# Optimization experiments

Hardware: AMD Instinct MI355X
Metric: run time of the kernel (lower is better)

The kernel has to match this reference:

```python
import jax, jax.numpy as jnp
import numpy as np

AZ = -999999.0  # ALMOST_ZERO_LOG_SCALE
N = 100000      # nodes
E = N - 1       # tree edges
D = 768         # input_dim
H = 256         # hidden_dim
C = 16          # num_classes


def setup_inputs() -> dict:
    key = jax.random.key(0)
    ks = jax.random.split(key, 14)
    scale = 0.02
    features = jax.random.normal(ks[0], (N, D), dtype=jnp.float32)
    # tree edges: child i (1..N-1) has parent sampled from [0, N)
    parent_idx = jax.random.randint(ks[1], (E,), 0, N, dtype=jnp.int32)
    child_idx = jnp.arange(1, N, dtype=jnp.int32)
    label_observed = jax.random.randint(ks[2], (N,), 0, 2, dtype=jnp.int32)
    true_labels = jax.random.randint(ks[3], (N,), 0, C, dtype=jnp.int32)
    # MLP feature extractor (num_layers=2, Linear+ReLU each, feature_extractor=True)
    W1 = jax.random.normal(ks[4], (D, H), dtype=jnp.float32) * scale
    b1 = jnp.zeros((H,), dtype=jnp.float32)
    W2 = jax.random.normal(ks[5], (H, H), dtype=jnp.float32) * scale
    b2 = jnp.zeros((H,), dtype=jnp.float32)
    # build_unary_potentials: Linear(H, C)
    Wu = jax.random.normal(ks[6], (H, C), dtype=jnp.float32) * scale
    bu = jnp.zeros((C,), dtype=jnp.float32)
    # build_edge_potentials: Linear(2H, C*C)
    We = jax.random.normal(ks[7], (2 * H, C * C), dtype=jnp.float32) * scale
    be = jnp.zeros((C * C,), dtype=jnp.float32)
    return {
        "features": features, "parent_idx": parent_idx, "child_idx": child_idx,
        "label_observed": label_observed, "true_labels": true_labels,
        "W1": W1, "b1": b1, "W2": W2, "b2": b2,
        "Wu": Wu, "bu": bu, "We": We, "be": be,
    }


def reference(features, parent_idx, child_idx, label_observed, true_labels,
              W1, b1, W2, b2, Wu, bu, We, be):
    obs = label_observed.astype(bool)
    # MLP feature extractor over all nodes at once (original loops per-node)
    h = jax.nn.relu(features @ W1 + b1)
    h = jax.nn.relu(h @ W2 + b2)                      # [N, H]
    # unary potentials; observed nodes get 0 at true label, AZ elsewhere
    unary_pred = h @ Wu + bu                          # [N, C]
    lbl = jnp.arange(C, dtype=true_labels.dtype)
    obs_unary = jnp.where(true_labels[:, None] == lbl[None, :], 0.0, AZ)
    unary = jnp.where(obs[:, None], obs_unary, unary_pred)  # [N, C]
    # edge potentials: Linear on concat(parent_hidden, child_hidden)
    hp = h[parent_idx]                                # [E, H]
    hc = h[child_idx]                                 # [E, H]
    ep = (jnp.concatenate([hp, hc], axis=1) @ We + be).reshape(E, C, C)
    pl = true_labels[parent_idx]                      # [E]
    cl = true_labels[child_idx]                       # [E]
    op = obs[parent_idx]                              # [E]
    oc = obs[child_idx]                               # [E]
    row = lbl[None, :, None]                          # broadcast over rows
    col = lbl[None, None, :]                          # broadcast over cols
    # both observed: 0 at [parent_label, child_label], AZ elsewhere
    allow_both = (row == pl[:, None, None]) & (col == cl[:, None, None])
    both = (op & oc)[:, None, None]
    # child-only observed: keep row at child label; parent-only: keep col at parent label
    keep = (((oc & ~op)[:, None, None] & (row == cl[:, None, None]))
            | ((op & ~oc)[:, None, None] & (col == pl[:, None, None]))
            | (~op & ~oc)[:, None, None])
    ep_masked = jnp.where(both,
                          jnp.where(allow_both, 0.0, AZ),
                          jnp.where(keep, ep, ep + AZ))
    return unary, ep_masked
```

## Files before the change

kernel.cpp:

```cpp
#include <hip/hip_runtime.h>
#include <cstddef>

#define AZ -999999.0f

typedef float  f32x4  __attribute__((ext_vector_type(4)));
typedef short  s16x8  __attribute__((ext_vector_type(8)));
typedef __bf16 bf16x8 __attribute__((ext_vector_type(8)));
typedef unsigned short ushort_t;

__device__ __forceinline__ ushort_t f2bf(float f) {
    return __builtin_bit_cast(ushort_t, (__bf16)f);
}

__device__ __forceinline__ f32x4 mfma16(s16x8 a, s16x8 b, f32x4 c) {
    return __builtin_amdgcn_mfma_f32_16x16x32_bf16(
        __builtin_bit_cast(bf16x8, a), __builtin_bit_cast(bf16x8, b), c, 0, 0, 0);
}

__device__ __forceinline__ void gl2lds16(const void* g, void* l) {
    __builtin_amdgcn_global_load_lds(
        (const __attribute__((address_space(1))) unsigned int*)g,
        (__attribute__((address_space(3))) unsigned int*)l, 16, 0, 0);
}

__global__ void setup_kernel(
    const float* __restrict__ W1, const float* __restrict__ W2,
    const float* __restrict__ We, const float* __restrict__ Wu,
    ushort_t* __restrict__ W1T, ushort_t* __restrict__ W2T,
    ushort_t* __restrict__ WeT, ushort_t* __restrict__ WuTs,
    const int* __restrict__ pidx, const int* __restrict__ cidx,
    const int* __restrict__ tl, const int* __restrict__ obs,
    int* __restrict__ meta, int E)
{
    int b = blockIdx.x, t = threadIdx.x;
    if (b < 768) {
        int idx = b * 256 + t; int k = idx >> 8, n = idx & 255;
        W1T[(size_t)n * 768 + k] = f2bf(W1[idx]);
    } else if (b < 1024) {
        int idx = (b - 768) * 256 + t; int k = idx >> 8, n = idx & 255;
        W2T[n * 256 + k] = f2bf(W2[idx]);
    } else if (b < 1536) {
        int idx = (b - 1024) * 256 + t; int k = idx >> 8, n = idx & 255;
        WeT[(size_t)n * 512 + k] = f2bf(We[idx]);
    } else if (b < 1552) {
        int idx = (b - 1536) * 256 + t; int k = idx >> 4, c = idx & 15;
        WuTs[c * 256 + (((k >> 3) ^ (c & 7)) << 3) + (k & 7)] = f2bf(Wu[idx]);
    } else {
        int e = (b - 1552) * 256 + t;
        if (e < E) {
            int p = pidx[e], c = cidx[e];
            meta[e] = (tl[p] & 15) | ((tl[c] & 15) << 4)
                    | ((obs[p] & 1) << 8) | ((obs[c] & 1) << 9);
        }
    }
}

template<int AMODE, int EPI>
__global__ __launch_bounds__(256) void gemm_kernel(
    const void* __restrict__ Aptr, const ushort_t* __restrict__ BT,
    const float* __restrict__ bias, void* __restrict__ outp,
    int M, int K,
    const int* __restrict__ parent_idx, const int* __restrict__ child_idx,
    const int* __restrict__ meta)
{
    constexpr int ABYTES = (AMODE == 0) ? 8192 : 4096;
    __shared__ __align__(16) char smem[ABYTES + 16384];
    float*    Asf = (float*)smem;
    ushort_t* Ash = (ushort_t*)smem;
    ushort_t* Bsh = (ushort_t*)(smem + ABYTES);

    const int tid  = threadIdx.x;
    const int lane = tid & 63, wave = tid >> 6;
    const int row0 = blockIdx.y * 64;
    const int wc   = wave * 64;
    const int quad = lane >> 4, l16 = lane & 15;
    const int c4   = lane & 3;

    const int rB  = tid >> 2;
    const int gcB = c4 ^ ((rB >> 1) & 3);
    size_t   b_off[4]; unsigned lds_b[4];
#pragma unroll
    for (int j = 0; j < 4; ++j) {
        b_off[j] = (size_t)(j * 64 + rB) * K + gcB * 8;
        lds_b[j] = (unsigned)(j * 64 + wave * 16) * 64;
    }

    size_t a_off[2]; unsigned lds_a[2];
    int pn = 0, cn = 0; unsigned lds_a0 = 0, a_col = 0;
    if constexpr (AMODE == 0) {
        const int c8 = tid & 7, r8 = tid >> 3;
        const int gcA = c8 ^ (r8 & 7);
#pragma unroll
        for (int j = 0; j < 2; ++j) {
            int gr = row0 + j * 32 + r8; if (gr > M - 1) gr = M - 1;
            a_off[j] = (size_t)gr * K + gcA * 4;
            lds_a[j] = (unsigned)(j * 32 + wave * 8) * 128;
        }
    } else {
        const int rA = tid >> 2;
        const int gcA2 = c4 ^ ((rA >> 1) & 3);
        int gr = row0 + rA; if (gr > M - 1) gr = M - 1;
        pn = parent_idx[gr]; cn = child_idx[gr];
        a_col  = gcA2 * 8;
        lds_a0 = (unsigned)(wave * 16) * 64;
    }

    const f32x4 fz = {0.f, 0.f, 0.f, 0.f};
    f32x4 acc[4][4];
#pragma unroll
    for (int i = 0; i < 4; ++i)
#pragma unroll
        for (int j = 0; j < 4; ++j) acc[i][j] = fz;

    const ushort_t* Abh = (const ushort_t*)Aptr;
    const float*    Af  = (const float*)Aptr;

    const int nkt = K >> 5;
    for (int kt = 0; kt < nkt; ++kt) {
        const int kbase = kt << 5;
        if constexpr (AMODE == 0) {
#pragma unroll
            for (int j = 0; j < 2; ++j)
                gl2lds16(Af + a_off[j] + kbase, smem + lds_a[j]);
        } else {
            int node = (kbase < 256) ? pn : cn;
            gl2lds16(Abh + (size_t)node * 256 + (kbase & 255) + a_col,
                     smem + lds_a0);
        }
#pragma unroll
        for (int j = 0; j < 4; ++j)
            gl2lds16(BT + b_off[j] + kbase, (char*)Bsh + lds_b[j]);

        __syncthreads();

        s16x8 af[4], bf[4];
        if constexpr (AMODE == 0) {
            const int s = l16 & 7;
            const int c0 = (2 * quad) ^ s, c1 = c0 ^ 1;
#pragma unroll
            for (int f = 0; f < 4; ++f) {
                int row = f * 16 + l16;
                f32x4 v0 = *(const f32x4*)&Asf[row * 32 + c0 * 4];
                f32x4 v1 = *(const f32x4*)&Asf[row * 32 + c1 * 4];
                s16x8 a;
                a[0] = (short)f2bf(v0[0]); a[1] = (short)f2bf(v0[1]);
                a[2] = (short)f2bf(v0[2]); a[3] = (short)f2bf(v0[3]);
                a[4] = (short)f2bf(v1[0]); a[5] = (short)f2bf(v1[1]);
                a[6] = (short)f2bf(v1[2]); a[7] = (short)f2bf(v1[3]);
                af[f] = a;
            }
        } else {
            const int ca = quad ^ ((l16 >> 1) & 3);
#pragma unroll
            for (int f = 0; f < 4; ++f)
                af[f] = *(const s16x8*)&Ash[(f * 16 + l16) * 32 + ca * 8];
        }
        {
            const int cb = quad ^ ((l16 >> 1) & 3);
#pragma unroll
            for (int f = 0; f < 4; ++f)
                bf[f] = *(const s16x8*)&Bsh[(wc + f * 16 + l16) * 32 + cb * 8];
        }
#pragma unroll
        for (int fr = 0; fr < 4; ++fr)
#pragma unroll
            for (int fc = 0; fc < 4; ++fc)
                acc[fr][fc] = mfma16(af[fr], bf[fc], acc[fr][fc]);
        __syncthreads();
    }

    float bv[4];
#pragma unroll
    for (int fc = 0; fc < 4; ++fc) bv[fc] = bias[wc + fc * 16 + l16];

    if constexpr (EPI == 0) {
        ushort_t* out = (ushort_t*)outp;
#pragma unroll
        for (int fr = 0; fr < 4; ++fr) {
#pragma unroll
            for (int r = 0; r < 4; ++r) {
                int gr = row0 + fr * 16 + quad * 4 + r;
                if (gr < M) {
#pragma unroll
                    for (int fc = 0; fc < 4; ++fc) {
                        float v = acc[fr][fc][r] + bv[fc];
                        v = v > 0.f ? v : 0.f;
                        out[(size_t)gr * 256 + wc + fc * 16 + l16] = f2bf(v);
                    }
                }
            }
        }
    } else {
        float* out = (float*)outp;
#pragma unroll
        for (int fr = 0; fr < 4; ++fr) {
#pragma unroll
            for (int r = 0; r < 4; ++r) {
                int e = row0 + fr * 16 + quad * 4 + r;
                if (e < M) {
                    int m  = meta[e];
                    int pl = m & 15, cl = (m >> 4) & 15;
                    int op = (m >> 8) & 1, oc = (m >> 9) & 1;
#pragma unroll
                    for (int fc = 0; fc < 4; ++fc) {
                        int n = wc + fc * 16 + l16;
                        float v = acc[fr][fc][r] + bv[fc];
                        int rr = n >> 4, cc = n & 15;
                        if (op & oc)  v = (rr == pl && cc == cl) ? 0.0f : AZ;
                        else if (oc)  { if (rr != cl) v += AZ; }
                        else if (op)  { if (cc != pl) v += AZ; }
                        out[(size_t)e * 256 + n] = v;
                    }
                }
            }
        }
    }
}

__global__ __launch_bounds__(256) void gemm2_unary_kernel(
    const ushort_t* __restrict__ h1, const ushort_t* __restrict__ W2T,
    const float* __restrict__ b2, const ushort_t* __restrict__ WuTs,
    const float* __restrict__ bu, const int* __restrict__ tl,
    const int* __restrict__ obs, ushort_t* __restrict__ h2,
    float* __restrict__ out_unary, int N)
{
    __shared__ __align__(16) char smem[4096 + 16384 + 32768 + 8192];
    ushort_t* Ash = (ushort_t*)smem;
    ushort_t* Bsh = (ushort_t*)(smem + 4096);
    ushort_t* Hsh = (ushort_t*)(smem + 20480);
    ushort_t* Wsh = (ushort_t*)(smem + 53248);

    const int tid = threadIdx.x, lane = tid & 63, wave = tid >> 6;
    const int quad = lane >> 4, l16 = lane & 15;
    const int sub4 = lane >> 2, c4 = lane & 3;
    const int n0 = blockIdx.x * 64;
    const int wc = wave * 64;

#pragma unroll
    for (int j = 0; j < 2; ++j)
        gl2lds16(WuTs + j * 2048 + wave * 512 + lane * 8,
                 (char*)Wsh + j * 4096 + wave * 1024);

    const int gcA = c4 ^ ((sub4 >> 1) & 3);
    int gra = n0 + wave * 16 + sub4; if (gra > N - 1) gra = N - 1;
    const size_t a_goff = (size_t)gra * 256 + gcA * 8;
    const unsigned a_loff = (unsigned)wave * 1024;
    size_t b_goff[4]; unsigned b_loff[4];
#pragma unroll
    for (int j = 0; j < 4; ++j) {
        int nrow = j * 64 + wave * 16 + sub4;
        b_goff[j] = (size_t)nrow * 256 + gcA * 8;
        b_loff[j] = (unsigned)(j * 64 + wave * 16) * 64;
    }

    const f32x4 fz = {0.f, 0.f, 0.f, 0.f};
    f32x4 acc[4][4];
#pragma unroll
    for (int i = 0; i < 4; ++i)
#pragma unroll
        for (int j = 0; j < 4; ++j) acc[i][j] = fz;

    for (int kt = 0; kt < 8; ++kt) {
        const int kbase = kt << 5;
        gl2lds16(h1 + a_goff + kbase, smem + a_loff);
#pragma unroll
        for (int j = 0; j < 4; ++j)
            gl2lds16(W2T + b_goff[j] + kbase, (char*)Bsh + b_loff[j]);
        __syncthreads();
        const int cs = quad ^ ((l16 >> 1) & 3);
        s16x8 af[4], bf[4];
#pragma unroll
        for (int f = 0; f < 4; ++f)
            af[f] = *(const s16x8*)&Ash[(f * 16 + l16) * 32 + cs * 8];
#pragma unroll
        for (int f = 0; f < 4; ++f)
            bf[f] = *(const s16x8*)&Bsh[(wc + f * 16 + l16) * 32 + cs * 8];
#pragma unroll
        for (int fr = 0; fr < 4; ++fr)
#pragma unroll
            for (int fc = 0; fc < 4; ++fc)
                acc[fr][fc] = mfma16(af[fr], bf[fc], acc[fr][fc]);
        __syncthreads();
    }

    float bv[4];
#pragma unroll
    for (int fc = 0; fc < 4; ++fc) bv[fc] = b2[wc + fc * 16 + l16];
#pragma unroll
    for (int fr = 0; fr < 4; ++fr) {
#pragma unroll
        for (int r = 0; r < 4; ++r) {
            int row = fr * 16 + quad * 4 + r;
#pragma unroll
            for (int fc = 0; fc < 4; ++fc) {
                int col = wc + fc * 16 + l16;
                float v = acc[fr][fc][r] + bv[fc];
                v = v > 0.f ? v : 0.f;
                Hsh[row * 256 + (((col >> 3) ^ (row & 7)) << 3) + (col & 7)] = f2bf(v);
            }
        }
    }
    __syncthreads();

    {
        int row = tid >> 2, cc = tid & 3;
        int gr = n0 + row;
        if (gr < N) {
#pragma unroll
            for (int j = 0; j < 8; ++j) {
                int phys = (j * 4 + cc) ^ (row & 7);
                s16x8 v = *(const s16x8*)&Hsh[row * 256 + phys * 8];
                *(s16x8*)&h2[(size_t)gr * 256 + (j * 4 + cc) * 8] = v;
            }
        }
    }

    {
        const int arow = wave * 16 + l16;
        f32x4 accu = fz;
#pragma unroll
        for (int kt = 0; kt < 8; ++kt) {
            int pc = (kt * 4 + quad) ^ (l16 & 7);
            s16x8 a = *(const s16x8*)&Hsh[arow * 256 + pc * 8];
            s16x8 b = *(const s16x8*)&Wsh[l16 * 256 + pc * 8];
            accu = mfma16(a, b, accu);
        }
        float bvc = bu[l16];
#pragma unroll
        for (int r = 0; r < 4; ++r) {
            int node = n0 + wave * 16 + quad * 4 + r;
            if (node < N) {
                float v = obs[node] ? ((tl[node] == l16) ? 0.0f : AZ) : (accu[r] + bvc);
                out_unary[(size_t)node * 16 + l16] = v;
            }
        }
    }
}

extern "C" void kernel_launch(void* const* d_in, const int* in_sizes, int n_in,
                              void* d_out, int out_size, void* d_ws, size_t ws_size,
                              hipStream_t stream) {
    const float* features = (const float*)d_in[0];
    const int* parent_idx = (const int*)d_in[1];
    const int* child_idx  = (const int*)d_in[2];
    const int* label_obs  = (const int*)d_in[3];
    const int* true_lab   = (const int*)d_in[4];
    const float* W1 = (const float*)d_in[5];
    const float* b1 = (const float*)d_in[6];
    const float* W2 = (const float*)d_in[7];
    const float* b2 = (const float*)d_in[8];
    const float* Wu = (const float*)d_in[9];
    const float* bu = (const float*)d_in[10];
    const float* We = (const float*)d_in[11];
    const float* be = (const float*)d_in[12];
    float* out = (float*)d_out;

    const int N = 100000, E = N - 1;

    char* ws = (char*)d_ws;
    ushort_t* h1   = (ushort_t*)ws;
    ushort_t* h2   = (ushort_t*)(ws + (size_t)N * 256 * 2);
    ushort_t* W1T  = (ushort_t*)(ws + (size_t)N * 256 * 4);
    ushort_t* W2T  = W1T + 768 * 256;
    ushort_t* WeT  = W2T + 256 * 256;
    ushort_t* WuTs = WeT + 512 * 256;
    int*      meta = (int*)(WuTs + 16 * 256);

    setup_kernel<<<1943, 256, 0, stream>>>(W1, W2, We, Wu, W1T, W2T, WeT, WuTs,
                                           parent_idx, child_idx, true_lab, label_obs,
                                           meta, E);

    dim3 gn(1, (N + 63) / 64);
    gemm_kernel<0, 0><<<gn, 256, 0, stream>>>(features, W1T, b1, h1, N, 768,
                                              nullptr, nullptr, nullptr);
    gemm2_unary_kernel<<<(N + 63) / 64, 256, 0, stream>>>(h1, W2T, b2, WuTs, bu,
                                                          true_lab, label_obs, h2, out, N);
    dim3 ge(1, (E + 63) / 64);
    gemm_kernel<2, 1><<<ge, 256, 0, stream>>>(h2, WeT, be, out + (size_t)N * 16, E, 512,
                                              parent_idx, child_idx, meta);
}
```

Baseline: 615.8 us.

## Fuse first MLP layer into node kernel, keep h1 in shared memory

Merges the features×W1 GEMM with the W2 GEMM and unary head into one node kernel, so the layer-1 activation stays in LDS instead of going through global memory. This removes one launch and the write and read of the N×256 bf16 h1 buffer. The trade-off is a 64KB LDS footprint per block, which limits occupancy, and no overlap between the layer-1 loads and the later stages.

```diff
diff --git a/kernel.cpp b/kernel.cpp
--- a/kernel.cpp
+++ b/kernel.cpp
@@ -55,185 +55,23 @@
     }
 }
 
-template<int AMODE, int EPI>
-__global__ __launch_bounds__(256) void gemm_kernel(
-    const void* __restrict__ Aptr, const ushort_t* __restrict__ BT,
-    const float* __restrict__ bias, void* __restrict__ outp,
-    int M, int K,
-    const int* __restrict__ parent_idx, const int* __restrict__ child_idx,
-    const int* __restrict__ meta)
-{
-    constexpr int ABYTES = (AMODE == 0) ? 8192 : 4096;
-    __shared__ __align__(16) char smem[ABYTES + 16384];
-    float*    Asf = (float*)smem;
-    ushort_t* Ash = (ushort_t*)smem;
-    ushort_t* Bsh = (ushort_t*)(smem + ABYTES);
-
-    const int tid  = threadIdx.x;
-    const int lane = tid & 63, wave = tid >> 6;
-    const int row0 = blockIdx.y * 64;
-    const int wc   = wave * 64;
-    const int quad = lane >> 4, l16 = lane & 15;
-    const int c4   = lane & 3;
-
-    const int rB  = tid >> 2;
-    const int gcB = c4 ^ ((rB >> 1) & 3);
-    size_t   b_off[4]; unsigned lds_b[4];
-#pragma unroll
-    for (int j = 0; j < 4; ++j) {
-        b_off[j] = (size_t)(j * 64 + rB) * K + gcB * 8;
-        lds_b[j] = (unsigned)(j * 64 + wave * 16) * 64;
-    }
-
-    size_t a_off[2]; unsigned lds_a[2];
-    int pn = 0, cn = 0; unsigned lds_a0 = 0, a_col = 0;
-    if constexpr (AMODE == 0) {
-        const int c8 = tid & 7, r8 = tid >> 3;
-        const int gcA = c8 ^ (r8 & 7);
-#pragma unroll
-        for (int j = 0; j < 2; ++j) {
-            int gr = row0 + j * 32 + r8; if (gr > M - 1) gr = M - 1;
-            a_off[j] = (size_t)gr * K + gcA * 4;
-            lds_a[j] = (unsigned)(j * 32 + wave * 8) * 128;
-        }
-    } else {
-        const int rA = tid >> 2;
-        const int gcA2 = c4 ^ ((rA >> 1) & 3);
-        int gr = row0 + rA; if (gr > M - 1) gr = M - 1;
-        pn = parent_idx[gr]; cn = child_idx[gr];
-        a_col  = gcA2 * 8;
-        lds_a0 = (unsigned)(wave * 16) * 64;
-    }
-
-    const f32x4 fz = {0.f, 0.f, 0.f, 0.f};
-    f32x4 acc[4][4];
-#pragma unroll
-    for (int i = 0; i < 4; ++i)
-#pragma unroll
-        for (int j = 0; j < 4; ++j) acc[i][j] = fz;
-
-    const ushort_t* Abh = (const ushort_t*)Aptr;
-    const float*    Af  = (const float*)Aptr;
-
-    const int nkt = K >> 5;
-    for (int kt = 0; kt < nkt; ++kt) {
-        const int kbase = kt << 5;
-        if constexpr (AMODE == 0) {
-#pragma unroll
-            for (int j = 0; j < 2; ++j)
-                gl2lds16(Af + a_off[j] + kbase, smem + lds_a[j]);
-        } else {
-            int node = (kbase < 256) ? pn : cn;
-            gl2lds16(Abh + (size_t)node * 256 + (kbase & 255) + a_col,
-                     smem + lds_a0);
-        }
-#pragma unroll
-        for (int j = 0; j < 4; ++j)
-            gl2lds16(BT + b_off[j] + kbase, (char*)Bsh + lds_b[j]);
-
-        __syncthreads();
-
-        s16x8 af[4], bf[4];
-        if constexpr (AMODE == 0) {
-            const int s = l16 & 7;
-            const int c0 = (2 * quad) ^ s, c1 = c0 ^ 1;
-#pragma unroll
-            for (int f = 0; f < 4; ++f) {
-                int row = f * 16 + l16;
-                f32x4 v0 = *(const f32x4*)&Asf[row * 32 + c0 * 4];
-                f32x4 v1 = *(const f32x4*)&Asf[row * 32 + c1 * 4];
-                s16x8 a;
-                a[0] = (short)f2bf(v0[0]); a[1] = (short)f2bf(v0[1]);
-                a[2] = (short)f2bf(v0[2]); a[3] = (short)f2bf(v0[3]);
-                a[4] = (short)f2bf(v1[0]); a[5] = (short)f2bf(v1[1]);
-                a[6] = (short)f2bf(v1[2]); a[7] = (short)f2bf(v1[3]);
-                af[f] = a;
-            }
-        } else {
-            const int ca = quad ^ ((l16 >> 1) & 3);
-#pragma unroll
-            for (int f = 0; f < 4; ++f)
-                af[f] = *(const s16x8*)&Ash[(f * 16 + l16) * 32 + ca * 8];
-        }
-        {
-            const int cb = quad ^ ((l16 >> 1) & 3);
-#pragma unroll
-            for (int f = 0; f < 4; ++f)
-                bf[f] = *(const s16x8*)&Bsh[(wc + f * 16 + l16) * 32 + cb * 8];
-        }
-#pragma unroll
-        for (int fr = 0; fr < 4; ++fr)
-#pragma unroll
-            for (int fc = 0; fc < 4; ++fc)
-                acc[fr][fc] = mfma16(af[fr], bf[fc], acc[fr][fc]);
-        __syncthreads();
-    }
-
-    float bv[4];
-#pragma unroll
-    for (int fc = 0; fc < 4; ++fc) bv[fc] = bias[wc + fc * 16 + l16];
-
-    if constexpr (EPI == 0) {
-        ushort_t* out = (ushort_t*)outp;
-#pragma unroll
-        for (int fr = 0; fr < 4; ++fr) {
-#pragma unroll
-            for (int r = 0; r < 4; ++r) {
-                int gr = row0 + fr * 16 + quad * 4 + r;
-                if (gr < M) {
-#pragma unroll
-                    for (int fc = 0; fc < 4; ++fc) {
-                        float v = acc[fr][fc][r] + bv[fc];
-                        v = v > 0.f ? v : 0.f;
-                        out[(size_t)gr * 256 + wc + fc * 16 + l16] = f2bf(v);
-                    }
-                }
-            }
-        }
-    } else {
-        float* out = (float*)outp;
-#pragma unroll
-        for (int fr = 0; fr < 4; ++fr) {
-#pragma unroll
-            for (int r = 0; r < 4; ++r) {
-                int e = row0 + fr * 16 + quad * 4 + r;
-                if (e < M) {
-                    int m  = meta[e];
-                    int pl = m & 15, cl = (m >> 4) & 15;
-                    int op = (m >> 8) & 1, oc = (m >> 9) & 1;
-#pragma unroll
-                    for (int fc = 0; fc < 4; ++fc) {
-                        int n = wc + fc * 16 + l16;
-                        float v = acc[fr][fc][r] + bv[fc];
-                        int rr = n >> 4, cc = n & 15;
-                        if (op & oc)  v = (rr == pl && cc == cl) ? 0.0f : AZ;
-                        else if (oc)  { if (rr != cl) v += AZ; }
-                        else if (op)  { if (cc != pl) v += AZ; }
-                        out[(size_t)e * 256 + n] = v;
-                    }
-                }
-            }
-        }
-    }
-}
-
-__global__ __launch_bounds__(256) void gemm2_unary_kernel(
-    const ushort_t* __restrict__ h1, const ushort_t* __restrict__ W2T,
+__global__ __launch_bounds__(256) void node_fused_kernel(
+    const float* __restrict__ features, const ushort_t* __restrict__ W1T,
+    const float* __restrict__ b1, const ushort_t* __restrict__ W2T,
     const float* __restrict__ b2, const ushort_t* __restrict__ WuTs,
     const float* __restrict__ bu, const int* __restrict__ tl,
     const int* __restrict__ obs, ushort_t* __restrict__ h2,
     float* __restrict__ out_unary, int N)
 {
-    __shared__ __align__(16) char smem[4096 + 16384 + 32768 + 8192];
-    ushort_t* Ash = (ushort_t*)smem;
-    ushort_t* Bsh = (ushort_t*)(smem + 4096);
-    ushort_t* Hsh = (ushort_t*)(smem + 20480);
-    ushort_t* Wsh = (ushort_t*)(smem + 53248);
+    __shared__ __align__(16) char smem[65536];
+    float*    Asf = (float*)smem;
+    ushort_t* Bsh = (ushort_t*)(smem + 8192);
+    ushort_t* Hsh = (ushort_t*)(smem + 24576);
+    ushort_t* Wsh = (ushort_t*)(smem + 57344);
 
     const int tid = threadIdx.x, lane = tid & 63, wave = tid >> 6;
     const int quad = lane >> 4, l16 = lane & 15;
-    const int sub4 = lane >> 2, c4 = lane & 3;
-    const int n0 = blockIdx.x * 64;
+    const int row0 = blockIdx.x * 64;
     const int wc = wave * 64;
 
 #pragma unroll
@@ -241,16 +79,20 @@
         gl2lds16(WuTs + j * 2048 + wave * 512 + lane * 8,
                  (char*)Wsh + j * 4096 + wave * 1024);
 
-    const int gcA = c4 ^ ((sub4 >> 1) & 3);
-    int gra = n0 + wave * 16 + sub4; if (gra > N - 1) gra = N - 1;
-    const size_t a_goff = (size_t)gra * 256 + gcA * 8;
-    const unsigned a_loff = (unsigned)wave * 1024;
-    size_t b_goff[4]; unsigned b_loff[4];
-#pragma unroll
-    for (int j = 0; j < 4; ++j) {
-        int nrow = j * 64 + wave * 16 + sub4;
-        b_goff[j] = (size_t)nrow * 256 + gcA * 8;
-        b_loff[j] = (unsigned)(j * 64 + wave * 16) * 64;
+    const int c4 = tid & 3, rB = tid >> 2;
+    const int gcB = c4 ^ ((rB >> 1) & 3);
+    unsigned lds_b[4];
+#pragma unroll
+    for (int j = 0; j < 4; ++j) lds_b[j] = (unsigned)(j * 64 + wave * 16) * 64;
+
+    const int c8 = tid & 7, r8 = tid >> 3;
+    const int gcA = c8 ^ (r8 & 7);
+    size_t a_off[2]; unsigned lds_a[2];
+#pragma unroll
+    for (int j = 0; j < 2; ++j) {
+        int gr = row0 + j * 32 + r8; if (gr > N - 1) gr = N - 1;
+        a_off[j] = (size_t)gr * 768 + gcA * 4;
+        lds_a[j] = (unsigned)(j * 32 + wave * 8) * 128;
     }
 
     const f32x4 fz = {0.f, 0.f, 0.f, 0.f};
@@ -260,21 +102,85 @@
 #pragma unroll
         for (int j = 0; j < 4; ++j) acc[i][j] = fz;
 
+    for (int kt = 0; kt < 24; ++kt) {
+        const int kbase = kt << 5;
+#pragma unroll
+        for (int j = 0; j < 2; ++j)
+            gl2lds16(features + a_off[j] + kbase, smem + lds_a[j]);
+#pragma unroll
+        for (int j = 0; j < 4; ++j)
+            gl2lds16(W1T + (size_t)(j * 64 + rB) * 768 + gcB * 8 + kbase,
+                     (char*)Bsh + lds_b[j]);
+        __syncthreads();
+
+        s16x8 af[4], bf[4];
+        const int s = l16 & 7;
+        const int c0 = (2 * quad) ^ s, c1 = c0 ^ 1;
+#pragma unroll
+        for (int f = 0; f < 4; ++f) {
+            int row = f * 16 + l16;
+            f32x4 v0 = *(const f32x4*)&Asf[row * 32 + c0 * 4];
+            f32x4 v1 = *(const f32x4*)&Asf[row * 32 + c1 * 4];
+            s16x8 a;
+            a[0] = (short)f2bf(v0[0]); a[1] = (short)f2bf(v0[1]);
+            a[2] = (short)f2bf(v0[2]); a[3] = (short)f2bf(v0[3]);
+            a[4] = (short)f2bf(v1[0]); a[5] = (short)f2bf(v1[1]);
+            a[6] = (short)f2bf(v1[2]); a[7] = (short)f2bf(v1[3]);
+            af[f] = a;
+        }
+        const int cb = quad ^ ((l16 >> 1) & 3);
+#pragma unroll
+        for (int f = 0; f < 4; ++f)
+            bf[f] = *(const s16x8*)&Bsh[(wc + f * 16 + l16) * 32 + cb * 8];
+#pragma unroll
+        for (int fr = 0; fr < 4; ++fr)
+#pragma unroll
+            for (int fc = 0; fc < 4; ++fc)
+                acc[fr][fc] = mfma16(af[fr], bf[fc], acc[fr][fc]);
+        __syncthreads();
+    }
+
+    {
+        float bv[4];
+#pragma unroll
+        for (int fc = 0; fc < 4; ++fc) bv[fc] = b1[wc + fc * 16 + l16];
+#pragma unroll
+        for (int fr = 0; fr < 4; ++fr) {
+#pragma unroll
+            for (int r = 0; r < 4; ++r) {
+                int row = fr * 16 + quad * 4 + r;
+#pragma unroll
+                for (int fc = 0; fc < 4; ++fc) {
+                    int col = wc + fc * 16 + l16;
+                    float v = acc[fr][fc][r] + bv[fc];
+                    v = v > 0.f ? v : 0.f;
+                    Hsh[row * 256 + (((col >> 3) ^ (row & 7)) << 3) + (col & 7)] = f2bf(v);
+                }
+            }
+        }
+    }
+#pragma unroll
+    for (int i = 0; i < 4; ++i)
+#pragma unroll
+        for (int j = 0; j < 4; ++j) acc[i][j] = fz;
+
     for (int kt = 0; kt < 8; ++kt) {
         const int kbase = kt << 5;
-        gl2lds16(h1 + a_goff + kbase, smem + a_loff);
 #pragma unroll
         for (int j = 0; j < 4; ++j)
-            gl2lds16(W2T + b_goff[j] + kbase, (char*)Bsh + b_loff[j]);
-        __syncthreads();
-        const int cs = quad ^ ((l16 >> 1) & 3);
+            gl2lds16(W2T + (size_t)(j * 64 + rB) * 256 + gcB * 8 + kbase,
+                     (char*)Bsh + lds_b[j]);
+        __syncthreads();
+
         s16x8 af[4], bf[4];
-#pragma unroll
-        for (int f = 0; f < 4; ++f)
-            af[f] = *(const s16x8*)&Ash[(f * 16 + l16) * 32 + cs * 8];
-#pragma unroll
-        for (int f = 0; f < 4; ++f)
-            bf[f] = *(const s16x8*)&Bsh[(wc + f * 16 + l16) * 32 + cs * 8];
+        const int pc = (kt * 4 + quad) ^ (l16 & 7);
+#pragma unroll
+        for (int f = 0; f < 4; ++f)
+            af[f] = *(const s16x8*)&Hsh[(f * 16 + l16) * 256 + pc * 8];
+        const int cb = quad ^ ((l16 >> 1) & 3);
+#pragma unroll
+        for (int f = 0; f < 4; ++f)
+            bf[f] = *(const s16x8*)&Bsh[(wc + f * 16 + l16) * 32 + cb * 8];
 #pragma unroll
         for (int fr = 0; fr < 4; ++fr)
 #pragma unroll
@@ -283,20 +189,22 @@
         __syncthreads();
     }
 
-    float bv[4];
-#pragma unroll
-    for (int fc = 0; fc < 4; ++fc) bv[fc] = b2[wc + fc * 16 + l16];
-#pragma unroll
-    for (int fr = 0; fr < 4; ++fr) {
-#pragma unroll
-        for (int r = 0; r < 4; ++r) {
-            int row = fr * 16 + quad * 4 + r;
-#pragma unroll
-            for (int fc = 0; fc < 4; ++fc) {
-                int col = wc + fc * 16 + l16;
-                float v = acc[fr][fc][r] + bv[fc];
-                v = v > 0.f ? v : 0.f;
-                Hsh[row * 256 + (((col >> 3) ^ (row & 7)) << 3) + (col & 7)] = f2bf(v);
+    {
+        float bv[4];
+#pragma unroll
+        for (int fc = 0; fc < 4; ++fc) bv[fc] = b2[wc + fc * 16 + l16];
+#pragma unroll
+        for (int fr = 0; fr < 4; ++fr) {
+#pragma unroll
+            for (int r = 0; r < 4; ++r) {
+                int row = fr * 16 + quad * 4 + r;
+#pragma unroll
+                for (int fc = 0; fc < 4; ++fc) {
+                    int col = wc + fc * 16 + l16;
+                    float v = acc[fr][fc][r] + bv[fc];
+                    v = v > 0.f ? v : 0.f;
+                    Hsh[row * 256 + (((col >> 3) ^ (row & 7)) << 3) + (col & 7)] = f2bf(v);
+                }
             }
         }
     }
@@ -304,7 +212,7 @@
 
     {
         int row = tid >> 2, cc = tid & 3;
-        int gr = n0 + row;
+        int gr = row0 + row;
         if (gr < N) {
 #pragma unroll
             for (int j = 0; j < 8; ++j) {
@@ -328,10 +236,102 @@
         float bvc = bu[l16];
 #pragma unroll
         for (int r = 0; r < 4; ++r) {
-            int node = n0 + wave * 16 + quad * 4 + r;
+            int node = row0 + wave * 16 + quad * 4 + r;
             if (node < N) {
                 float v = obs[node] ? ((tl[node] == l16) ? 0.0f : AZ) : (accu[r] + bvc);
                 out_unary[(size_t)node * 16 + l16] = v;
+            }
+        }
+    }
+}
+
+__global__ __launch_bounds__(256) void edge_gemm_kernel(
+    const ushort_t* __restrict__ h2, const ushort_t* __restrict__ WeT,
+    const float* __restrict__ bias, float* __restrict__ out,
+    int M,
+    const int* __restrict__ parent_idx, const int* __restrict__ child_idx,
+    const int* __restrict__ meta)
+{
+    __shared__ __align__(16) char smem[4096 + 16384];
+    ushort_t* Ash = (ushort_t*)smem;
+    ushort_t* Bsh = (ushort_t*)(smem + 4096);
+
+    const int tid  = threadIdx.x;
+    const int lane = tid & 63, wave = tid >> 6;
+    const int row0 = blockIdx.x * 64;
+    const int wc   = wave * 64;
+    const int quad = lane >> 4, l16 = lane & 15;
+    const int c4   = tid & 3, rB = tid >> 2;
+
+    const int gcB = c4 ^ ((rB >> 1) & 3);
+    size_t   b_off[4]; unsigned lds_b[4];
+#pragma unroll
+    for (int j = 0; j < 4; ++j) {
+        b_off[j] = (size_t)(j * 64 + rB) * 512 + gcB * 8;
+        lds_b[j] = (unsigned)(j * 64 + wave * 16) * 64;
+    }
+
+    int gr = row0 + rB; if (gr > M - 1) gr = M - 1;
+    const int pn = parent_idx[gr], cn = child_idx[gr];
+    const unsigned a_col  = (unsigned)gcB * 8;
+    const unsigned lds_a0 = (unsigned)(wave * 16) * 64;
+
+    const f32x4 fz = {0.f, 0.f, 0.f, 0.f};
+    f32x4 acc[4][4];
+#pragma unroll
+    for (int i = 0; i < 4; ++i)
+#pragma unroll
+        for (int j = 0; j < 4; ++j) acc[i][j] = fz;
+
+    for (int kt = 0; kt < 16; ++kt) {
+        const int kbase = kt << 5;
+        int node = (kbase < 256) ? pn : cn;
+        gl2lds16(h2 + (size_t)node * 256 + (kbase & 255) + a_col, smem + lds_a0);
+#pragma unroll
+        for (int j = 0; j < 4; ++j)
+            gl2lds16(WeT + b_off[j] + kbase, (char*)Bsh + lds_b[j]);
+
+        __syncthreads();
+
+        s16x8 af[4], bf[4];
+        const int ca = quad ^ ((l16 >> 1) & 3);
+#pragma unroll
+        for (int f = 0; f < 4; ++f)
+            af[f] = *(const s16x8*)&Ash[(f * 16 + l16) * 32 + ca * 8];
+#pragma unroll
+        for (int f = 0; f < 4; ++f)
+            bf[f] = *(const s16x8*)&Bsh[(wc + f * 16 + l16) * 32 + ca * 8];
+#pragma unroll
+        for (int fr = 0; fr < 4; ++fr)
+#pragma unroll
+            for (int fc = 0; fc < 4; ++fc)
+                acc[fr][fc] = mfma16(af[fr], bf[fc], acc[fr][fc]);
+        __syncthreads();
+    }
+
+    float bv[4];
+#pragma unroll
+    for (int fc = 0; fc < 4; ++fc) bv[fc] = bias[wc + fc * 16 + l16];
+
+#pragma unroll
+    for (int fr = 0; fr < 4; ++fr) {
+#pragma unroll
+        for (int r = 0; r < 4; ++r) {
+            int e = row0 + fr * 16 + quad * 4 + r;
+            if (e < M) {
+                int m  = meta[e];
+                int pl = m & 15, cl = (m >> 4) & 15;
+                int op = (m >> 8) & 1, oc = (m >> 9) & 1;
+#pragma unroll
+                for (int fc = 0; fc < 4; ++fc) {
+                    int n = wc + fc * 16 + l16;
+                    float v = acc[fr][fc][r] + bv[fc];
+                    int rr = n >> 4, cc = n & 15;
+                    if (op & oc)  v = (rr == pl && cc == cl) ? 0.0f : AZ;
+                    else if (oc)  { if (rr != cl) v += AZ; }
+                    else if (op)  { if (cc != pl) v += AZ; }
+                    out[(size_t)e * 256 + n] = v;
+                }
             }
         }
     }
@@ -358,9 +358,8 @@
     const int N = 100000, E = N - 1;
 
     char* ws = (char*)d_ws;
-    ushort_t* h1   = (ushort_t*)ws;
-    ushort_t* h2   = (ushort_t*)(ws + (size_t)N * 256 * 2);
-    ushort_t* W1T  = (ushort_t*)(ws + (size_t)N * 256 * 4);
+    ushort_t* h2   = (ushort_t*)ws;
+    ushort_t* W1T  = (ushort_t*)(ws + (size_t)N * 256 * 2);
     ushort_t* W2T  = W1T + 768 * 256;
     ushort_t* WeT  = W2T + 256 * 256;
     ushort_t* WuTs = WeT + 512 * 256;
@@ -370,12 +369,9 @@
                                            parent_idx, child_idx, true_lab, label_obs,
                                            meta, E);
 
-    dim3 gn(1, (N + 63) / 64);
-    gemm_kernel<0, 0><<<gn, 256, 0, stream>>>(features, W1T, b1, h1, N, 768,
-                                              nullptr, nullptr, nullptr);
-    gemm2_unary_kernel<<<(N + 63) / 64, 256, 0, stream>>>(h1, W2T, b2, WuTs, bu,
-                                                          true_lab, label_obs, h2, out, N);
-    dim3 ge(1, (E + 63) / 64);
-    gemm_kernel<2, 1><<<ge, 256, 0, stream>>>(h2, WeT, be, out + (size_t)N * 16, E, 512,
-                                              parent_idx, child_idx, meta);
-}
+    node_fused_kernel<<<(N + 63) / 64, 256, 0, stream>>>(
+        features, W1T, b1, W2T, b2, WuTs, bu, true_lab, label_obs, h2, out, N);
+
+    edge_gemm_kernel<<<(E + 63) / 64, 256, 0, stream>>>(
+        h2, WeT, be, out + (size_t)N * 16, E, parent_idx, child_idx, meta);
+}
```

Result: no change. 608.7 us (-1.2%).
